# Performance work log

Measured on AMD Instinct MI355X. Metric: run time of the kernel, lower is better.

The kernel has to match this reference:

```python
import jax, jax.numpy as jnp
import numpy as np
import math

T, B, I, H, L = 1024, 64, 512, 512, 2


def setup_inputs() -> dict:
    key = jax.random.key(0)
    ks = jax.random.split(key, 16)
    s = 1.0 / math.sqrt(H)
    inp = {
        "x": jax.random.normal(ks[0], (T, B, I), jnp.float32),
        "h0": jax.random.normal(ks[1], (L, B, H), jnp.float32),
        "c0": jax.random.normal(ks[2], (L, B, H), jnp.float32),
    }
    names = ["w_ih_0", "w_hh_0", "b_ih_0", "b_hh_0", "w_ih_1", "w_hh_1", "b_ih_1", "b_hh_1"]
    shapes = [(4 * H, I), (4 * H, H), (4 * H,), (4 * H,), (4 * H, H), (4 * H, H), (4 * H,), (4 * H,)]
    for i, (n, sh) in enumerate(zip(names, shapes)):
        inp[n] = jax.random.normal(ks[3 + i], sh, jnp.float32) * s
    return inp


def _lstm_layer(x, h0, c0, w_ih, w_hh, b_ih, b_hh):
    # x: [T,B,in]; h0,c0: [B,H].  NOTE: original module re-reads the INITIAL
    # (h0,c0) at every timestep (no temporal recurrence), so this vectorizes over T.
    hh = h0 @ w_hh.T + b_hh                          # [B,4H], same for all t
    gates = jnp.einsum('tbi,gi->tbg', x, w_ih) + b_ih + hh[None]  # [T,B,4H]
    i_g, f_g, g_g, o_g = jnp.split(gates, 4, axis=-1)
    cy = jax.nn.sigmoid(f_g) * c0[None] + jax.nn.sigmoid(i_g) * jnp.tanh(g_g)
    hy = jax.nn.sigmoid(o_g) * jnp.tanh(cy)
    return hy, cy                                     # [T,B,H] each


def reference(x, h0, c0, w_ih_0, w_hh_0, b_ih_0, b_hh_0, w_ih_1, w_hh_1, b_ih_1, b_hh_1):
    params = [(w_ih_0, w_hh_0, b_ih_0, b_hh_0), (w_ih_1, w_hh_1, b_ih_1, b_hh_1)]
    cur = x
    last_h, last_c = [], []
    for l in range(L):
        hy, cy = _lstm_layer(cur, h0[l], c0[l], *params[l])
        last_h.append(hy[-1])
        last_c.append(cy[-1])
        cur = hy
    t, b, h = cur.shape
    result = cur.reshape(t * b, 1, h)  # == torch.cat over time then unsqueeze(1)
    return result, jnp.stack(last_h), jnp.stack(last_c)
```

## Files before the change

kernel.cpp:

```cpp
#include <hip/hip_runtime.h>
#include <hip/hip_bf16.h>

#define T_DIM 1024
#define B_DIM 64
#define H_DIM 512

typedef __attribute__((ext_vector_type(8))) short short8;
typedef __attribute__((ext_vector_type(4))) float f32x4;

typedef __attribute__((address_space(3))) void lds_void_t;
typedef __attribute__((address_space(1))) void glob_void_t;

static __device__ __forceinline__ unsigned short f2b_rne(float f) {
  unsigned u = __float_as_uint(f);
  u += 0x7fffu + ((u >> 16) & 1u);
  return (unsigned short)(u >> 16);
}

static __device__ __forceinline__ float sigm(float x) {
  return 1.0f / (1.0f + __expf(-x));
}
static __device__ __forceinline__ float tanh_fast(float x) {
  float e = __expf(2.0f * fabsf(x));
  float t = 1.0f - 2.0f / (e + 1.0f);
  return copysignf(t, x);
}

__global__ void conv_f2b(const float* __restrict__ in,
                         unsigned short* __restrict__ out, int n4) {
  int idx = blockIdx.x * blockDim.x + threadIdx.x;
  int stride = gridDim.x * blockDim.x;
  for (int i = idx; i < n4; i += stride) {
    float4 v = reinterpret_cast<const float4*>(in)[i];
    ushort4 o;
    o.x = f2b_rne(v.x); o.y = f2b_rne(v.y);
    o.z = f2b_rne(v.z); o.w = f2b_rne(v.w);
    reinterpret_cast<ushort4*>(out)[i] = o;
  }
}

__global__ void hh_bias(const float* __restrict__ h0,
                        const float* __restrict__ whh0, const float* __restrict__ whh1,
                        const float* __restrict__ bih0, const float* __restrict__ bhh0,
                        const float* __restrict__ bih1, const float* __restrict__ bhh1,
                        float* __restrict__ hhb) {
  const int l = blockIdx.y;
  const int wid = threadIdx.x >> 6;
  const int lane = threadIdx.x & 63;
  const int g = blockIdx.x * 4 + wid;
  const float* wh = l ? whh1 : whh0;
  const float* bi = l ? bih1 : bih0;
  const float* bh = l ? bhh1 : bhh0;
  const float4* wr = reinterpret_cast<const float4*>(wh + (size_t)g * H_DIM);
  float4 w0 = wr[lane * 2];
  float4 w1 = wr[lane * 2 + 1];
  float bias = bi[g] + bh[g];
  const float* h0l = h0 + (size_t)l * B_DIM * H_DIM;
  for (int b = 0; b < B_DIM; ++b) {
    const float4* hr = reinterpret_cast<const float4*>(h0l + (size_t)b * H_DIM);
    float4 a0 = hr[lane * 2];
    float4 a1 = hr[lane * 2 + 1];
    float acc = a0.x * w0.x + a0.y * w0.y + a0.z * w0.z + a0.w * w0.w +
                a1.x * w1.x + a1.y * w1.y + a1.z * w1.z + a1.w * w1.w;
#pragma unroll
    for (int off = 32; off; off >>= 1) acc += __shfl_xor(acc, off);
    if (lane == 0) hhb[((size_t)l * B_DIM + b) * 2048 + g] = acc + bias;
  }
}

template <int LAYER>
__global__ __launch_bounds__(256, 2) void lstm_gemm(
    const unsigned short* __restrict__ Abf,
    const unsigned short* __restrict__ Wbf,
    const float* __restrict__ hhb,
    const float* __restrict__ c0l,
    unsigned short* __restrict__ hy_bf,
    float* __restrict__ out_hy,
    float* __restrict__ out_lasth,
    float* __restrict__ out_lastc) {
  __shared__ __attribute__((aligned(16))) unsigned short Alds[128 * 64];
  __shared__ __attribute__((aligned(16))) unsigned short Blds[128 * 64];

  const int tid = threadIdx.x;
  const int lane = tid & 63;
  const int wid = tid >> 6;
  const int wr = wid >> 1, wc = wid & 1;

  const int lin = blockIdx.x;
  const int wg = (lin & 7) * 1024 + (lin >> 3);
  const int bh = wg & 15;
  const int bm = wg >> 4;
  const int m0 = bm * 128;
  const int h0v = bh * 32;
  const int lane_lo = lane & 15, lane_hi = lane >> 4;
  const int srow = tid >> 3;
  const int slot = tid & 7;

  f32x4 acc[4][4] = {};

  for (int ks = 0; ks < 8; ++ks) {
    const int k0 = ks * 64;
#pragma unroll
    for (int i = 0; i < 4; ++i) {
      int row = i * 32 + srow;
      int sch = slot ^ (row & 7);
      const unsigned short* src = Abf + (size_t)(m0 + row) * 512 + k0 + sch * 8;
      char* dst = (char*)Alds + i * 4096 + wid * 1024;
      __builtin_amdgcn_global_load_lds((const glob_void_t*)src, (lds_void_t*)dst, 16, 0, 0);
    }
#pragma unroll
    for (int i = 0; i < 4; ++i) {
      int n = i * 32 + srow;
      int sch = slot ^ (n & 7);
      int wrow = (n >> 5) * H_DIM + h0v + (n & 31);
      const unsigned short* src = Wbf + (size_t)wrow * 512 + k0 + sch * 8;
      char* dst = (char*)Blds + i * 4096 + wid * 1024;
      __builtin_amdgcn_global_load_lds((const glob_void_t*)src, (lds_void_t*)dst, 16, 0, 0);
    }
    __syncthreads();

#pragma unroll
    for (int kk = 0; kk < 2; ++kk) {
      const int cbase = kk * 4 + lane_hi;
      short8 aF[4];
#pragma unroll
      for (int r = 0; r < 4; ++r) {
        int row = wr * 64 + r * 16 + lane_lo;
        aF[r] = *reinterpret_cast<const short8*>(
            (const char*)Alds + row * 128 + ((cbase ^ (row & 7)) << 4));
      }
      short8 bF[4];
#pragma unroll
      for (int g = 0; g < 4; ++g) {
        int n = g * 32 + wc * 16 + lane_lo;
        bF[g] = *reinterpret_cast<const short8*>(
            (const char*)Blds + n * 128 + ((cbase ^ (n & 7)) << 4));
      }
#pragma unroll
      for (int r = 0; r < 4; ++r)
#pragma unroll
        for (int g = 0; g < 4; ++g)
          acc[r][g] = __builtin_amdgcn_mfma_f32_16x16x32_bf16(aF[r], bF[g], acc[r][g], 0, 0, 0);
    }
    __syncthreads();
  }

  const int h = h0v + wc * 16 + lane_lo;
#pragma unroll
  for (int r = 0; r < 4; ++r) {
#pragma unroll
    for (int j = 0; j < 4; ++j) {
      int m = m0 + wr * 64 + r * 16 + lane_hi * 4 + j;
      int b = m & (B_DIM - 1);
      bool isLast = (m >> 6) == (T_DIM - 1);
      const float* hb = hhb + (size_t)b * 2048;
      float gi = acc[r][0][j] + hb[h];
      float gf = acc[r][1][j] + hb[512 + h];
      float gg = acc[r][2][j] + hb[1024 + h];
      float go = acc[r][3][j] + hb[1536 + h];
      float iv = sigm(gi), fv = sigm(gf), gv = tanh_fast(gg), ov = sigm(go);
      float cv = fv * c0l[b * H_DIM + h] + iv * gv;
      float hv = ov * tanh_fast(cv);
      if (LAYER == 0) {
        hy_bf[(size_t)m * H_DIM + h] = f2b_rne(hv);
      } else {
        out_hy[(size_t)m * H_DIM + h] = hv;
      }
      if (isLast) {
        out_lasth[b * H_DIM + h] = hv;
        out_lastc[b * H_DIM + h] = cv;
      }
    }
  }
}

extern "C" void kernel_launch(void* const* d_in, const int* in_sizes, int n_in,
                              void* d_out, int out_size, void* d_ws, size_t ws_size,
                              hipStream_t stream) {
  const float* x    = (const float*)d_in[0];
  const float* h0   = (const float*)d_in[1];
  const float* c0   = (const float*)d_in[2];
  const float* wih0 = (const float*)d_in[3];
  const float* whh0 = (const float*)d_in[4];
  const float* bih0 = (const float*)d_in[5];
  const float* bhh0 = (const float*)d_in[6];
  const float* wih1 = (const float*)d_in[7];
  const float* whh1 = (const float*)d_in[8];
  const float* bih1 = (const float*)d_in[9];
  const float* bhh1 = (const float*)d_in[10];
  float* out = (float*)d_out;

  char* ws = (char*)d_ws;
  unsigned short* x_bf   = (unsigned short*)(ws);
  unsigned short* hy0_bf = (unsigned short*)(ws + 67108864);
  unsigned short* w0_bf  = (unsigned short*)(ws + 134217728);
  unsigned short* w1_bf  = (unsigned short*)(ws + 136314880);
  float*          hhb    = (float*)(ws + 138412032);

  conv_f2b<<<2048, 256, 0, stream>>>(x, x_bf, 33554432 / 4);
  conv_f2b<<<512, 256, 0, stream>>>(wih0, w0_bf, 1048576 / 4);
  conv_f2b<<<512, 256, 0, stream>>>(wih1, w1_bf, 1048576 / 4);
  hh_bias<<<dim3(512, 2), 256, 0, stream>>>(h0, whh0, whh1, bih0, bhh0, bih1, bhh1, hhb);

  float* res   = out;
  float* lasth = out + 33554432;
  float* lastc = out + 33554432 + 65536;

  lstm_gemm<0><<<8192, 256, 0, stream>>>(
      x_bf, w0_bf, hhb, c0, hy0_bf, nullptr, lasth, lastc);
  lstm_gemm<1><<<8192, 256, 0, stream>>>(
      hy0_bf, w1_bf, hhb + 64 * 2048, c0 + 64 * 512, nullptr, res,
      lasth + 64 * 512, lastc + 64 * 512);
}
```

Baseline: 674.9 us.

## Enlarge LSTM GEMM tiles to 256x256 with double-buffered LDS and ping-pong scheduling

Replaces the 128x128 tile, single-buffer GEMM with a 256x256 tile (64 hidden units times 4 gates) computed by 512 threads. The K loop stages the next k-slice into a second LDS buffer with global_load_lds and waits on vmcnt. MFMA work is split into four quadrants separated by barriers and s_setprio to overlap LDS reads and global loads with compute. The aim is more data reuse per tile and hidden load latency, at the cost of 128KB of LDS, many more accumulator registers and fewer blocks.

After: 738.8 us. 1.09x slower.

```diff
diff --git a/kernel.cpp b/kernel.cpp
--- a/kernel.cpp
+++ b/kernel.cpp
@@ -69,7 +69,7 @@
 }
 
 template <int LAYER>
-__global__ __launch_bounds__(256, 2) void lstm_gemm(
+__global__ __launch_bounds__(512, 2) void lstm_gemm(
     const unsigned short* __restrict__ Abf,
     const unsigned short* __restrict__ Wbf,
     const float* __restrict__ hhb,
@@ -78,79 +78,159 @@
     float* __restrict__ out_hy,
     float* __restrict__ out_lasth,
     float* __restrict__ out_lastc) {
-  __shared__ __attribute__((aligned(16))) unsigned short Alds[128 * 64];
-  __shared__ __attribute__((aligned(16))) unsigned short Blds[128 * 64];
+  __shared__ __attribute__((aligned(16))) unsigned short Alds[2][256 * 64];
+  __shared__ __attribute__((aligned(16))) unsigned short Blds[2][256 * 64];
 
   const int tid = threadIdx.x;
   const int lane = tid & 63;
   const int wid = tid >> 6;
-  const int wr = wid >> 1, wc = wid & 1;
+  const int wm = wid >> 2, wn = wid & 3;
+  const int lane_lo = lane & 15, lane_hi = lane >> 4;
 
   const int lin = blockIdx.x;
-  const int wg = (lin & 7) * 1024 + (lin >> 3);
-  const int bh = wg & 15;
-  const int bm = wg >> 4;
-  const int m0 = bm * 128;
-  const int h0v = bh * 32;
-  const int lane_lo = lane & 15, lane_hi = lane >> 4;
-  const int srow = tid >> 3;
+  const int wg = (lin & 7) * 256 + (lin >> 3);
+  const int bn = wg & 7;
+  const int bm = wg >> 3;
+  const int m0 = bm * 256;
+  const int h0v = bn * 64;
+
+  const int rowh = tid >> 3;
   const int slot = tid & 7;
-
-  f32x4 acc[4][4] = {};
-
-  for (int ks = 0; ks < 8; ++ks) {
-    const int k0 = ks * 64;
-#pragma unroll
-    for (int i = 0; i < 4; ++i) {
-      int row = i * 32 + srow;
-      int sch = slot ^ (row & 7);
-      const unsigned short* src = Abf + (size_t)(m0 + row) * 512 + k0 + sch * 8;
-      char* dst = (char*)Alds + i * 4096 + wid * 1024;
-      __builtin_amdgcn_global_load_lds((const glob_void_t*)src, (lds_void_t*)dst, 16, 0, 0);
-    }
-#pragma unroll
-    for (int i = 0; i < 4; ++i) {
-      int n = i * 32 + srow;
-      int sch = slot ^ (n & 7);
-      int wrow = (n >> 5) * H_DIM + h0v + (n & 31);
-      const unsigned short* src = Wbf + (size_t)wrow * 512 + k0 + sch * 8;
-      char* dst = (char*)Blds + i * 4096 + wid * 1024;
-      __builtin_amdgcn_global_load_lds((const glob_void_t*)src, (lds_void_t*)dst, 16, 0, 0);
-    }
-    __syncthreads();
-
-#pragma unroll
-    for (int kk = 0; kk < 2; ++kk) {
-      const int cbase = kk * 4 + lane_hi;
-      short8 aF[4];
-#pragma unroll
-      for (int r = 0; r < 4; ++r) {
-        int row = wr * 64 + r * 16 + lane_lo;
-        aF[r] = *reinterpret_cast<const short8*>(
-            (const char*)Alds + row * 128 + ((cbase ^ (row & 7)) << 4));
-      }
-      short8 bF[4];
-#pragma unroll
-      for (int g = 0; g < 4; ++g) {
-        int n = g * 32 + wc * 16 + lane_lo;
-        bF[g] = *reinterpret_cast<const short8*>(
-            (const char*)Blds + n * 128 + ((cbase ^ (n & 7)) << 4));
-      }
-#pragma unroll
-      for (int r = 0; r < 4; ++r)
-#pragma unroll
-        for (int g = 0; g < 4; ++g)
-          acc[r][g] = __builtin_amdgcn_mfma_f32_16x16x32_bf16(aF[r], bF[g], acc[r][g], 0, 0, 0);
-    }
-    __syncthreads();
-  }
-
-  const int h = h0v + wc * 16 + lane_lo;
-#pragma unroll
-  for (int r = 0; r < 4; ++r) {
+  const int csch = slot ^ (rowh & 7);
+
+  const unsigned short* pA = Abf + (size_t)(m0 + rowh) * 512 + csch * 8;
+  const unsigned short* pB =
+      Wbf + (size_t)((rowh >> 4) * 512 + h0v + (rowh & 15)) * 512 + csch * 8;
+
+  char* aldsB = (char*)&Alds[0][0];
+  char* bldsB = (char*)&Blds[0][0];
+  const int dstBase = wid * 1024;
+
+#define STAGE_A(bb, kt, ha)                                                   \
+  {                                                                           \
+    __builtin_amdgcn_global_load_lds(                                         \
+        (const glob_void_t*)(pA + (size_t)(ha)*65536 + (kt)*64),              \
+        (lds_void_t*)(aldsB + (bb)*32768 + (ha)*16384 + dstBase), 16, 0, 0);  \
+    __builtin_amdgcn_global_load_lds(                                         \
+        (const glob_void_t*)(pA + (size_t)(ha)*65536 + 32768 + (kt)*64),      \
+        (lds_void_t*)(aldsB + (bb)*32768 + (ha)*16384 + 8192 + dstBase), 16,  \
+        0, 0);                                                                \
+  }
+#define STAGE_B(bb, kt, hb)                                                   \
+  {                                                                           \
+    __builtin_amdgcn_global_load_lds(                                         \
+        (const glob_void_t*)(pB + (size_t)((hb)*2) * 8192 + (kt)*64),         \
+        (lds_void_t*)(bldsB + (bb)*32768 + (hb)*16384 + dstBase), 16, 0, 0);  \
+    __builtin_amdgcn_global_load_lds(                                         \
+        (const glob_void_t*)(pB + (size_t)((hb)*2 + 1) * 8192 + (kt)*64),     \
+        (lds_void_t*)(bldsB + (bb)*32768 + (hb)*16384 + 8192 + dstBase), 16,  \
+        0, 0);                                                                \
+  }
+
+  int cx0 = ((0 * 4 + lane_hi) ^ (lane_lo & 7)) << 4;
+  int cx1 = ((1 * 4 + lane_hi) ^ (lane_lo & 7)) << 4;
+  const int aRow = (wm * 128 + lane_lo) * 128;
+  const int bRow = (wn * 64 + lane_lo) * 128;
+#define A_ADDR(bb, r, cx) (aldsB + (bb)*32768 + aRow + (r)*2048 + (cx))
+#define B_ADDR(bb, g, cx) (bldsB + (bb)*32768 + bRow + (g)*2048 + (cx))
+#define LD8(p) (*reinterpret_cast<const short8*>(p))
+
+  f32x4 acc[8][4] = {};
+  short8 aF[4][2], bF[2][2];
+
+  STAGE_A(0, 0, 0); STAGE_A(0, 0, 1);
+  STAGE_B(0, 0, 0); STAGE_B(0, 0, 1);
+
+#pragma unroll
+  for (int kt = 0; kt < 8; ++kt) {
+    const int cur = kt & 1, nxt = cur ^ 1;
+    if (kt < 7) { STAGE_A(nxt, kt + 1, 0); STAGE_A(nxt, kt + 1, 1); }
+    if (kt < 7) {
+      asm volatile("s_waitcnt vmcnt(4)" ::: "memory");
+    } else {
+      asm volatile("s_waitcnt vmcnt(0)" ::: "memory");
+    }
+    __builtin_amdgcn_s_barrier();
+#pragma unroll
+    for (int r = 0; r < 4; ++r) {
+      aF[r][0] = LD8(A_ADDR(cur, r, cx0));
+      aF[r][1] = LD8(A_ADDR(cur, r, cx1));
+    }
+#pragma unroll
+    for (int g = 0; g < 2; ++g) {
+      bF[g][0] = LD8(B_ADDR(cur, g, cx0));
+      bF[g][1] = LD8(B_ADDR(cur, g, cx1));
+    }
+    __builtin_amdgcn_s_barrier();
+    __builtin_amdgcn_s_setprio(1);
+#pragma unroll
+    for (int r = 0; r < 4; ++r)
+#pragma unroll
+      for (int g = 0; g < 2; ++g) {
+        acc[r][g] = __builtin_amdgcn_mfma_f32_16x16x32_bf16(aF[r][0], bF[g][0], acc[r][g], 0, 0, 0);
+        acc[r][g] = __builtin_amdgcn_mfma_f32_16x16x32_bf16(aF[r][1], bF[g][1], acc[r][g], 0, 0, 0);
+      }
+    __builtin_amdgcn_s_setprio(0);
+#pragma unroll
+    for (int g = 0; g < 2; ++g) {
+      bF[g][0] = LD8(B_ADDR(cur, 2 + g, cx0));
+      bF[g][1] = LD8(B_ADDR(cur, 2 + g, cx1));
+    }
+    if (kt < 7) { STAGE_B(nxt, kt + 1, 0); STAGE_B(nxt, kt + 1, 1); }
+    __builtin_amdgcn_s_barrier();
+    __builtin_amdgcn_s_setprio(1);
+#pragma unroll
+    for (int r = 0; r < 4; ++r)
+#pragma unroll
+      for (int g = 0; g < 2; ++g) {
+        acc[r][2 + g] = __builtin_amdgcn_mfma_f32_16x16x32_bf16(aF[r][0], bF[g][0], acc[r][2 + g], 0, 0, 0);
+        acc[r][2 + g] = __builtin_amdgcn_mfma_f32_16x16x32_bf16(aF[r][1], bF[g][1], acc[r][2 + g], 0, 0, 0);
+      }
+    __builtin_amdgcn_s_setprio(0);
+#pragma unroll
+    for (int r = 0; r < 4; ++r) {
+      aF[r][0] = LD8(A_ADDR(cur, 4 + r, cx0));
+      aF[r][1] = LD8(A_ADDR(cur, 4 + r, cx1));
+    }
+#pragma unroll
+    for (int g = 0; g < 2; ++g) {
+      bF[g][0] = LD8(B_ADDR(cur, g, cx0));
+      bF[g][1] = LD8(B_ADDR(cur, g, cx1));
+    }
+    __builtin_amdgcn_s_barrier();
+    __builtin_amdgcn_s_setprio(1);
+#pragma unroll
+    for (int r = 0; r < 4; ++r)
+#pragma unroll
+      for (int g = 0; g < 2; ++g) {
+        acc[4 + r][g] = __builtin_amdgcn_mfma_f32_16x16x32_bf16(aF[r][0], bF[g][0], acc[4 + r][g], 0, 0, 0);
+        acc[4 + r][g] = __builtin_amdgcn_mfma_f32_16x16x32_bf16(aF[r][1], bF[g][1], acc[4 + r][g], 0, 0, 0);
+      }
+    __builtin_amdgcn_s_setprio(0);
+#pragma unroll
+    for (int g = 0; g < 2; ++g) {
+      bF[g][0] = LD8(B_ADDR(cur, 2 + g, cx0));
+      bF[g][1] = LD8(B_ADDR(cur, 2 + g, cx1));
+    }
+    __builtin_amdgcn_s_barrier();
+    __builtin_amdgcn_s_setprio(1);
+#pragma unroll
+    for (int r = 0; r < 4; ++r)
+#pragma unroll
+      for (int g = 0; g < 2; ++g) {
+        acc[4 + r][2 + g] = __builtin_amdgcn_mfma_f32_16x16x32_bf16(aF[r][0], bF[g][0], acc[4 + r][2 + g], 0, 0, 0);
+        acc[4 + r][2 + g] = __builtin_amdgcn_mfma_f32_16x16x32_bf16(aF[r][1], bF[g][1], acc[4 + r][2 + g], 0, 0, 0);
+      }
+    __builtin_amdgcn_s_setprio(0);
+    __builtin_amdgcn_s_barrier();
+  }
+
+  const int h = h0v + wn * 16 + lane_lo;
+#pragma unroll
+  for (int r = 0; r < 8; ++r) {
 #pragma unroll
     for (int j = 0; j < 4; ++j) {
-      int m = m0 + wr * 64 + r * 16 + lane_hi * 4 + j;
+      int m = m0 + wm * 128 + r * 16 + lane_hi * 4 + j;
       int b = m & (B_DIM - 1);
       bool isLast = (m >> 6) == (T_DIM - 1);
       const float* hb = hhb + (size_t)b * 2048;
@@ -172,6 +252,11 @@
       }
     }
   }
+#undef STAGE_A
+#undef STAGE_B
+#undef A_ADDR
+#undef B_ADDR
+#undef LD8
 }
 
 extern "C" void kernel_launch(void* const* d_in, const int* in_sizes, int n_in,
@@ -206,9 +291,9 @@
   float* lasth = out + 33554432;
   float* lastc = out + 33554432 + 65536;
 
-  lstm_gemm<0><<<8192, 256, 0, stream>>>(
+  lstm_gemm<0><<<2048, 512, 0, stream>>>(
       x_bf, w0_bf, hhb, c0, hy0_bf, nullptr, lasth, lastc);
-  lstm_gemm<1><<<8192, 256, 0, stream>>>(
+  lstm_gemm<1><<<2048, 512, 0, stream>>>(
       hy0_bf, w1_bf, hhb + 64 * 2048, c0 + 64 * 512, nullptr, res,
       lasth + 64 * 512, lastc + 64 * 512);
 }
```
